# Kernel optimization log

Hardware: AMD Instinct MI355X
Metric: run time of the kernel (lower is better)

The kernel has to match this reference:

```python
import jax, jax.numpy as jnp
import numpy as np


def setup_inputs() -> dict:
    key = jax.random.key(0)
    k1, k2 = jax.random.split(key)
    data = jax.random.normal(k1, (16, 64, 128, 128), dtype=jnp.float32)
    weights = jax.random.normal(k2, (128, 64, 3, 3), dtype=jnp.float32)
    return {"data": data, "weights": weights}


def reference(data, weights):
    # Original module performs im2col (unfold+reshape) + matmul, which is
    # mathematically a stride-1 VALID cross-correlation in NCHW layout.
    # weights: [C_out, C_in, kH, kW]; output: [B, C_out, H-kH+1, W-kW+1]
    return jax.lax.conv_general_dilated(
        data, weights,
        window_strides=(1, 1),
        padding="VALID",
        dimension_numbers=("NCHW", "OIHW", "NCHW"),
    )
```

## Files before the change

### kernel.cpp

```cpp
#include <hip/hip_runtime.h>


#define BATCH 16
#define CIN   64
#define HIN   128
#define WIN   128
#define COUT  128
#define HO    126
#define WO    126

typedef short bf16x8 __attribute__((ext_vector_type(8)));
typedef float f32x4  __attribute__((ext_vector_type(4)));

__device__ __forceinline__ unsigned short f2bf(float f) {
    union { float f; unsigned int u; } v; v.f = f;
    unsigned int u = v.u;
    unsigned int r = (u + 0x7fffu + ((u >> 16) & 1u)) >> 16;
    return (unsigned short)r;
}

__device__ __forceinline__ void async16(const void* g, void* l) {
    __builtin_amdgcn_global_load_lds(
        (const __attribute__((address_space(1))) unsigned int*)(unsigned long long)g,
        (__attribute__((address_space(3))) unsigned int*)(unsigned long long)l,
        16, 0, 0);
}

__global__ __launch_bounds__(256) void t2_weights(
        const float* __restrict__ w, unsigned short* __restrict__ wt) {
    const int idx = blockIdx.x * 256 + threadIdx.x;
    if (idx < COUT * CIN * 9) {
        const int co = idx / (CIN * 9);
        const int r  = idx % (CIN * 9);
        const int ci = r / 9;
        const int k  = r % 9;
        wt[((size_t)k * COUT + co) * CIN + ci] = f2bf(w[idx]);
    }
}

__global__ __launch_bounds__(512, 4) void conv_fused(
        const float* __restrict__ x,
        const unsigned short* __restrict__ wt,
        float* __restrict__ out) {
    __shared__ __align__(16) char smem[26112 + 32768 + 9520];
    short* halo = (short*)smem;
    short* As   = (short*)(smem + 26112);
    unsigned short* tile = (unsigned short*)(smem + 26112 + 32768);

    const int raw = (blockIdx.z * 126 + blockIdx.y) * 2 + blockIdx.x;
    const int s = (raw & 7) * 504 + (raw >> 3);
    const int b  = s / 252;
    const int r2 = s - b * 252;
    const int oh = r2 >> 1;
    const int W0 = (r2 & 1) * 64;

    const int tid  = threadIdx.x;
    const int lane = tid & 63, wid = tid >> 6;
    const int co0  = (wid & 3) * 32;
    const int n0   = (wid >> 2) * 32;
    const int col  = lane & 15, quad = lane >> 4;
    const int swl = (lane * 16) ^ ((lane >> 3) << 4);

    {
        const char* srcA = (const char*)wt;
        char* dstA = (char*)As;
#pragma unroll
        for (int i = 0; i < 2; i++) {
            const int c = wid * 2 + i;
            async16(srcA + c * 1024 + swl, dstA + c * 1024 + lane * 16);
        }
    }

    for (int kh = 0; kh < 3; kh++) {
        const int h = oh + kh;
        {
            const int w4 = (tid & 15) * 4, cib = tid >> 4;
#pragma unroll
            for (int j = 0; j < 2; j++) {
                const int ci = cib + 32 * j;
                f32x4 v = *(const f32x4*)&x[(((size_t)b * CIN + ci) * HIN + h) * WIN + W0 + w4];
#pragma unroll
                for (int q = 0; q < 4; q++)
                    tile[(w4 + q) * 70 + ci] = f2bf(v[q]);
            }
            if (W0 == 0 && tid < 256) {
                const int w = 64 + (tid & 3), ci = tid >> 2;
                tile[w * 70 + ci] = f2bf(x[(((size_t)b * CIN + ci) * HIN + h) * WIN + w]);
            }
        }
        __syncthreads();
        {
            const int ci4 = (tid & 15) * 4, wr = tid >> 4;
#pragma unroll
            for (int jj = 0; jj < 3; jj++) {
                const int widx = wr + 32 * jj;
                if (jj < 2 || wr < 4) {
                    ushort4 v = *(const ushort4*)&tile[widx * 70 + ci4];
                    const int r = kh * 68 + widx;
                    *(ushort4*)((char*)halo + ((r * 128 + ci4 * 2) ^ ((r & 7) << 4))) = v;
                }
            }
        }
        __syncthreads();
    }

    f32x4 acc[2][2] = {};

#pragma unroll
    for (int t = 0; t < 9; t++) {
        const int kh = t / 3, kw = t - kh * 3;
        if (t + 1 < 9) {
            const char* srcA = (const char*)wt + (size_t)(t + 1) * 16384;
            char* dstA = (char*)As + ((t + 1) & 1) * 16384;
#pragma unroll
            for (int i = 0; i < 2; i++) {
                const int c = wid * 2 + i;
                async16(srcA + c * 1024 + swl, dstA + c * 1024 + lane * 16);
            }
        }
        const short* At = As + (t & 1) * 8192;
#pragma unroll
        for (int kk = 0; kk < 2; kk++) {
            bf16x8 aa[2], bb[2];
#pragma unroll
            for (int mi = 0; mi < 2; mi++) {
                const int r = co0 + mi * 16 + col;
                aa[mi] = *(const bf16x8*)&At[(r * 64 + kk * 32 + quad * 8) ^ ((r & 7) << 3)];
            }
#pragma unroll
            for (int ni = 0; ni < 2; ni++) {
                const int r = kh * 68 + n0 + ni * 16 + col + kw;
                bb[ni] = *(const bf16x8*)&halo[(r * 64 + kk * 32 + quad * 8) ^ ((r & 7) << 3)];
            }
#pragma unroll
            for (int mi = 0; mi < 2; mi++)
#pragma unroll
                for (int ni = 0; ni < 2; ni++)
                    acc[mi][ni] = __builtin_amdgcn_mfma_f32_16x16x32_bf16(
                        aa[mi], bb[ni], acc[mi][ni], 0, 0, 0);
        }
        if (t + 1 < 9) __syncthreads();
    }

#pragma unroll
    for (int ni = 0; ni < 2; ni++) {
        const int ow = W0 + n0 + ni * 16 + col;
        if (ow < WO) {
#pragma unroll
            for (int mi = 0; mi < 2; mi++) {
                const int co = co0 + mi * 16 + quad * 4;
                float* o = out + (((size_t)b * COUT + co) * HO + oh) * WO + ow;
#pragma unroll
                for (int r = 0; r < 4; r++)
                    o[(size_t)r * HO * WO] = acc[mi][ni][r];
            }
        }
    }
}

__global__ __launch_bounds__(256) void conv_direct(
        const float* __restrict__ x, const float* __restrict__ w,
        float* __restrict__ y) {
    const int idx = blockIdx.x * 256 + threadIdx.x;
    if (idx >= BATCH * COUT * HO * WO) return;
    const int ow = idx % WO;
    int t = idx / WO;
    const int oh = t % HO; t /= HO;
    const int co = t % COUT;
    const int b  = t / COUT;
    float acc = 0.f;
    const float* xb = x + (((size_t)b * CIN) * HIN + oh) * WIN + ow;
    const float* wc = w + (size_t)co * (CIN * 9);
    for (int ci = 0; ci < CIN; ci++) {
#pragma unroll
        for (int kh = 0; kh < 3; kh++)
#pragma unroll
            for (int kw = 0; kw < 3; kw++)
                acc += xb[(size_t)ci * (HIN * WIN) + kh * WIN + kw] * wc[ci * 9 + kh * 3 + kw];
    }
    y[idx] = acc;
}

extern "C" void kernel_launch(void* const* d_in, const int* in_sizes, int n_in,
                              void* d_out, int out_size, void* d_ws, size_t ws_size,
                              hipStream_t stream) {
    const float* data    = (const float*)d_in[0];
    const float* weights = (const float*)d_in[1];
    float* out = (float*)d_out;

    const size_t wt_bytes = (size_t)9 * COUT * CIN * 2;

    if (ws_size >= wt_bytes) {
        unsigned short* wt = (unsigned short*)d_ws;
        t2_weights<<<(COUT * CIN * 9 + 255) / 256, 256, 0, stream>>>(weights, wt);
        conv_fused<<<dim3(2, 126, BATCH), 512, 0, stream>>>(data, wt, out);
    } else {
        const int n = BATCH * COUT * HO * WO;
        conv_direct<<<(n + 255) / 256, 256, 0, stream>>>(data, weights, out);
    }
}
```

Baseline: 237.9 us.

## Build halo tile directly from registers, dropping staging tile and barriers

Each thread now loads 8 channels × 3 rows of one column into registers with scalar coalesced loads. It converts them to bf16 and writes a packed 16-byte vector straight into the swizzled halo, so the transposing staging tile and five of the six barriers go away. All global loads are issued up front, before the weight prefetch, which raises memory-level parallelism. The cost is more registers per thread (24+8 floats) and scalar rather than float4 global loads. The clamped right-edge load may fetch duplicate data.

```diff
diff --git a/kernel.cpp b/kernel.cpp
--- a/kernel.cpp
+++ b/kernel.cpp
@@ -42,10 +42,9 @@
         const float* __restrict__ x,
         const unsigned short* __restrict__ wt,
         float* __restrict__ out) {
-    __shared__ __align__(16) char smem[26112 + 32768 + 9520];
+    __shared__ __align__(16) char smem[26112 + 32768];
     short* halo = (short*)smem;
     short* As   = (short*)(smem + 26112);
-    unsigned short* tile = (unsigned short*)(smem + 26112 + 32768);
 
     const int raw = (blockIdx.z * 126 + blockIdx.y) * 2 + blockIdx.x;
     const int s = (raw & 7) * 504 + (raw >> 3);
@@ -61,6 +60,28 @@
     const int col  = lane & 15, quad = lane >> 4;
     const int swl = (lane * 16) ^ ((lane >> 3) << 4);
 
+    const int tw = tid & 63, oct = tid >> 6;
+    float v[3][8];
+    {
+        const float* xb = x + ((size_t)b * CIN + oct * 8) * (HIN * WIN)
+                            + (size_t)oh * WIN + W0 + tw;
+#pragma unroll
+        for (int kh = 0; kh < 3; kh++)
+#pragma unroll
+            for (int j = 0; j < 8; j++)
+                v[kh][j] = xb[(size_t)j * (HIN * WIN) + kh * WIN];
+    }
+    float tv[8];
+    const int oct2 = tid & 7, tw2 = 64 + ((tid >> 3) & 3), tkh = tid >> 5;
+    if (tid < 96) {
+        int wi = W0 + tw2; if (wi > WIN - 1) wi = WIN - 1;
+        const float* xb2 = x + ((size_t)b * CIN + oct2 * 8) * (HIN * WIN)
+                             + (size_t)(oh + tkh) * WIN + wi;
+#pragma unroll
+        for (int j = 0; j < 8; j++)
+            tv[j] = xb2[(size_t)j * (HIN * WIN)];
+    }
+
     {
         const char* srcA = (const char*)wt;
         char* dstA = (char*)As;
@@ -71,38 +92,23 @@
         }
     }
 
+#pragma unroll
     for (int kh = 0; kh < 3; kh++) {
-        const int h = oh + kh;
-        {
-            const int w4 = (tid & 15) * 4, cib = tid >> 4;
-#pragma unroll
-            for (int j = 0; j < 2; j++) {
-                const int ci = cib + 32 * j;
-                f32x4 v = *(const f32x4*)&x[(((size_t)b * CIN + ci) * HIN + h) * WIN + W0 + w4];
-#pragma unroll
-                for (int q = 0; q < 4; q++)
-                    tile[(w4 + q) * 70 + ci] = f2bf(v[q]);
-            }
-            if (W0 == 0 && tid < 256) {
-                const int w = 64 + (tid & 3), ci = tid >> 2;
-                tile[w * 70 + ci] = f2bf(x[(((size_t)b * CIN + ci) * HIN + h) * WIN + w]);
-            }
-        }
-        __syncthreads();
-        {
-            const int ci4 = (tid & 15) * 4, wr = tid >> 4;
-#pragma unroll
-            for (int jj = 0; jj < 3; jj++) {
-                const int widx = wr + 32 * jj;
-                if (jj < 2 || wr < 4) {
-                    ushort4 v = *(const ushort4*)&tile[widx * 70 + ci4];
-                    const int r = kh * 68 + widx;
-                    *(ushort4*)((char*)halo + ((r * 128 + ci4 * 2) ^ ((r & 7) << 4))) = v;
-                }
-            }
-        }
-        __syncthreads();
-    }
+        bf16x8 p;
+#pragma unroll
+        for (int j = 0; j < 8; j++) p[j] = (short)f2bf(v[kh][j]);
+        const int r = kh * 68 + tw;
+        *(bf16x8*)((char*)halo + ((r * 128 + oct * 16) ^ ((r & 7) << 4))) = p;
+    }
+    if (tid < 96) {
+        bf16x8 p;
+#pragma unroll
+        for (int j = 0; j < 8; j++) p[j] = (short)f2bf(tv[j]);
+        const int r = tkh * 68 + tw2;
+        *(bf16x8*)((char*)halo + ((r * 128 + oct2 * 16) ^ ((r & 7) << 4))) = p;
+    }
+
+    __syncthreads();
 
     f32x4 acc[2][2] = {};
 
```

New measurement: 232.1 us. -2.4%, faster.
